# Optimization experiments

Hardware: AMD Instinct MI355X
Metric: run time of the kernel (lower is better)

Reference implementation:

```python
import jax, jax.numpy as jnp
import numpy as np

B, C, T = 8, 256, 4096
IC = C // 2  # inter_channels
BN_EPS = 1e-5


def setup_inputs() -> dict:
    key = jax.random.key(0)
    ks = jax.random.split(key, 12)
    s_in = 1.0 / np.sqrt(C)
    s_ic = 1.0 / np.sqrt(IC)
    return {
        "x": jax.random.normal(ks[0], (B, C, T), dtype=jnp.float32),
        "theta_w": jax.random.uniform(ks[1], (IC, C), jnp.float32, -s_in, s_in),
        "theta_b": jax.random.uniform(ks[2], (IC,), jnp.float32, -s_in, s_in),
        "phi_w": jax.random.uniform(ks[3], (IC, C), jnp.float32, -s_in, s_in),
        "phi_b": jax.random.uniform(ks[4], (IC,), jnp.float32, -s_in, s_in),
        "g_w": jax.random.uniform(ks[5], (IC, C), jnp.float32, -s_in, s_in),
        "g_b": jax.random.uniform(ks[6], (IC,), jnp.float32, -s_in, s_in),
        "w_w": jax.random.uniform(ks[7], (C, IC), jnp.float32, -s_ic, s_ic),
        "w_b": jax.random.uniform(ks[8], (C,), jnp.float32, -s_ic, s_ic),
        "bn_gamma": jax.random.normal(ks[9], (C,), dtype=jnp.float32),
        "bn_beta": jax.random.normal(ks[10], (C,), dtype=jnp.float32),
    }


def _conv1x1(w, b, inp):
    # Conv1d kernel_size=1 == per-position channel matmul
    return jnp.einsum('oc,bct->bot', w, inp) + b[None, :, None]


def _maxpool2(z):
    b, c, t = z.shape
    return z.reshape(b, c, t // 2, 2).max(axis=-1)


def reference(x, theta_w, theta_b, phi_w, phi_b, g_w, g_b, w_w, w_b, bn_gamma, bn_beta):
    theta_x = _conv1x1(theta_w, theta_b, x)              # (B, IC, T)
    phi_x = _maxpool2(_conv1x1(phi_w, phi_b, x))         # (B, IC, T/2)
    g_x = _maxpool2(_conv1x1(g_w, g_b, x))               # (B, IC, T/2)

    # f = theta^T @ phi ; softmax-free, divided by N = T/2
    f = jnp.einsum('bct,bcs->bts', theta_x, phi_x)       # (B, T, T/2)
    f_div_C = f / f.shape[-1]
    y = jnp.einsum('bts,bcs->bct', f_div_C, g_x)         # (B, IC, T)

    w_y = _conv1x1(w_w, w_b, y)                          # (B, C, T)
    # BatchNorm1d (training-mode batch statistics over batch+time)
    mean = w_y.mean(axis=(0, 2), keepdims=True)
    var = w_y.var(axis=(0, 2), keepdims=True)
    w_y = (w_y - mean) * jax.lax.rsqrt(var + BN_EPS)
    w_y = w_y * bn_gamma[None, :, None] + bn_beta[None, :, None]
    return w_y + x
```

## Files before the change

### kernel.cpp

```cpp
#include <hip/hip_runtime.h>
#include <hip/hip_bf16.h>

typedef __attribute__((ext_vector_type(8))) short short8;
typedef __attribute__((ext_vector_type(4))) short short4v;
typedef __attribute__((ext_vector_type(4))) float floatx4;
typedef unsigned int u32;

#define BB 8
#define CC 256
#define ICH 128
#define TT 4096
#define SS 2048
static constexpr float BN_EPS = 1e-5f;
static constexpr float INV_S  = 1.0f / 2048.0f;
static constexpr float INV_BT = 1.0f / 32768.0f;

typedef const __attribute__((address_space(1))) u32* gas_ptr;
typedef __attribute__((address_space(3))) u32* las_ptr;
__device__ __forceinline__ void gl_lds16(const void* g, void* l) {
    __builtin_amdgcn_global_load_lds((gas_ptr)g, (las_ptr)l, 16, 0, 0);
}

__global__ __launch_bounds__(256) void k0x_transpose(
    const float* __restrict__ x, __hip_bfloat16* __restrict__ xt,
    const float* __restrict__ phi_w, const float* __restrict__ g_w,
    __hip_bfloat16* __restrict__ Wf)
{
    if (blockIdx.z == 8) {
        if (blockIdx.y != 0) return;
        int idx = blockIdx.x * 256 + threadIdx.x;
        const float* src = (idx < 8192) ? (phi_w + (size_t)idx * 4)
                                        : (g_w + (size_t)(idx - 8192) * 4);
        float4 v = *(const float4*)src;
        alignas(8) __hip_bfloat16 t[4];
        t[0] = __float2bfloat16(v.x); t[1] = __float2bfloat16(v.y);
        t[2] = __float2bfloat16(v.z); t[3] = __float2bfloat16(v.w);
        *(short4v*)(Wf + (size_t)idx * 4) = *(const short4v*)t;
        return;
    }

    __shared__ float Tl[64][65];
    const int b = blockIdx.z, cb = blockIdx.y * 64, tb = blockIdx.x * 64;
    const int tid = threadIdx.x;
    #pragma unroll
    for (int it = 0; it < 4; ++it) {
        int idx = tid + 256 * it;
        int row = idx >> 4, c4 = idx & 15;
        float4 v = *(const float4*)(x + ((size_t)b * CC + cb + row) * TT + tb + c4 * 4);
        Tl[row][c4 * 4 + 0] = v.x; Tl[row][c4 * 4 + 1] = v.y;
        Tl[row][c4 * 4 + 2] = v.z; Tl[row][c4 * 4 + 3] = v.w;
    }
    __syncthreads();
    #pragma unroll
    for (int it = 0; it < 2; ++it) {
        int idx = tid + 256 * it;
        int trow = idx >> 3, ch = idx & 7;
        alignas(16) __hip_bfloat16 tmp[8];
        #pragma unroll
        for (int e = 0; e < 8; ++e) tmp[e] = __float2bfloat16(Tl[ch * 8 + e][trow]);
        *(short8*)(xt + ((size_t)b * TT + tb + trow) * CC + cb + ch * 8) = *(const short8*)tmp;
    }
}

__global__ __launch_bounds__(256) void k1_mfma(
    const __hip_bfloat16* __restrict__ Wf, const float* __restrict__ phi_b,
    const float* __restrict__ g_b, const __hip_bfloat16* __restrict__ xt,
    __hip_bfloat16* __restrict__ phi_g)
{
    __shared__ short lds[128 * 132];
    short* As = lds;
    short* Bs = lds + 128 * 64;

    const int b  = blockIdx.z;
    const int m0 = blockIdx.y * 128;
    const int tb = blockIdx.x * 128;
    const int s0 = blockIdx.x * 64;
    const int tid = threadIdx.x;
    const int w = tid >> 6, l = tid & 63;
    const int quad = l >> 4, lm = l & 15;
    const int wm = (w & 1) * 64, wn = (w >> 1) * 64;
    const int rs = l >> 3, cs = (l & 7) * 8;

    const __hip_bfloat16* Ap = Wf + (size_t)m0 * CC;
    const __hip_bfloat16* Bp = xt + ((size_t)b * TT + tb) * CC;

    floatx4 acc[4][4];
    #pragma unroll
    for (int i = 0; i < 4; ++i)
        #pragma unroll
        for (int j = 0; j < 4; ++j) acc[i][j] = (floatx4)0.f;

    for (int kc = 0; kc < 4; ++kc) {
        const int k0 = kc * 64;
        const int rbase = w * 32;
        #pragma unroll
        for (int t = 0; t < 4; ++t) {
            gl_lds16(Ap + (size_t)(rbase + t * 8 + rs) * CC + k0 + cs, &As[(rbase + t * 8) * 64]);
            gl_lds16(Bp + (size_t)(rbase + t * 8 + rs) * CC + k0 + cs, &Bs[(rbase + t * 8) * 64]);
        }
        __syncthreads();
        #pragma unroll
        for (int ks = 0; ks < 2; ++ks) {
            short8 a[4], bb[4];
            #pragma unroll
            for (int i = 0; i < 4; ++i)
                a[i] = *(const short8*)&As[(wm + i * 16 + lm) * 64 + ks * 32 + quad * 8];
            #pragma unroll
            for (int j = 0; j < 4; ++j)
                bb[j] = *(const short8*)&Bs[(wn + j * 16 + lm) * 64 + ks * 32 + quad * 8];
            #pragma unroll
            for (int i = 0; i < 4; ++i)
                #pragma unroll
                for (int j = 0; j < 4; ++j)
                    acc[i][j] = __builtin_amdgcn_mfma_f32_16x16x32_bf16(a[i], bb[j], acc[i][j], 0, 0, 0);
        }
        __syncthreads();
    }

    __hip_bfloat16* Out = (__hip_bfloat16*)lds;
    #pragma unroll
    for (int i = 0; i < 4; ++i)
        #pragma unroll
        for (int j = 0; j < 4; ++j)
            #pragma unroll
            for (int r = 0; r < 4; ++r)
                Out[(wm + i * 16 + quad * 4 + r) * 132 + wn + j * 16 + lm] =
                    __float2bfloat16(acc[i][j][r]);
    __syncthreads();
    #pragma unroll
    for (int it = 0; it < 4; ++it) {
        int idx = tid + 256 * it;
        int orow = idx >> 3, grp = idx & 7;
        int o = m0 + orow;
        float bias = (o < ICH) ? phi_b[o] : g_b[o - ICH];
        short8 v0 = *(const short8*)&Out[orow * 132 + grp * 16];
        short8 v1 = *(const short8*)&Out[orow * 132 + grp * 16 + 8];
        const __hip_bfloat16* p0 = (const __hip_bfloat16*)&v0;
        const __hip_bfloat16* p1 = (const __hip_bfloat16*)&v1;
        alignas(16) __hip_bfloat16 o8[8];
        #pragma unroll
        for (int e = 0; e < 4; ++e)
            o8[e] = __float2bfloat16(
                fmaxf(__bfloat162float(p0[2 * e]), __bfloat162float(p0[2 * e + 1])) + bias);
        #pragma unroll
        for (int e = 0; e < 4; ++e)
            o8[4 + e] = __float2bfloat16(
                fmaxf(__bfloat162float(p1[2 * e]), __bfloat162float(p1[2 * e + 1])) + bias);
        *(short8*)(phi_g + ((size_t)b * CC + o) * SS + s0 + grp * 8) = *(const short8*)o8;
    }
}

__global__ __launch_bounds__(256) void k2_mfma(
    const __hip_bfloat16* __restrict__ phi_g, float* __restrict__ Mpart)
{
    __shared__ short lds[2 * 128 * 64];
    short* As = lds;
    short* Bs = lds + 128 * 64;
    const int sc = blockIdx.x, b = blockIdx.y;
    const int tid = threadIdx.x;
    const int w = tid >> 6, l = tid & 63;
    const int quad = l >> 4, lm = l & 15;
    const int wm = (w & 1) * 64, wn = (w >> 1) * 64;
    const int rs = l >> 3, cs = (l & 7) * 8;

    const __hip_bfloat16* Ap = phi_g + (size_t)b * CC * SS + sc * 512;
    const __hip_bfloat16* Bp = Ap + (size_t)ICH * SS;

    floatx4 acc[4][4];
    #pragma unroll
    for (int i = 0; i < 4; ++i)
        #pragma unroll
        for (int j = 0; j < 4; ++j) acc[i][j] = (floatx4)0.f;

    for (int kc = 0; kc < 8; ++kc) {
        const int k0 = kc * 64;
        const int rbase = w * 32;
        #pragma unroll
        for (int t = 0; t < 4; ++t) {
            gl_lds16(Ap + (size_t)(rbase + t * 8 + rs) * SS + k0 + cs, &As[(rbase + t * 8) * 64]);
            gl_lds16(Bp + (size_t)(rbase + t * 8 + rs) * SS + k0 + cs, &Bs[(rbase + t * 8) * 64]);
        }
        __syncthreads();
        #pragma unroll
        for (int ks = 0; ks < 2; ++ks) {
            short8 a[4], bb[4];
            #pragma unroll
            for (int i = 0; i < 4; ++i)
                a[i] = *(const short8*)&As[(wm + i * 16 + lm) * 64 + ks * 32 + quad * 8];
            #pragma unroll
            for (int j = 0; j < 4; ++j)
                bb[j] = *(const short8*)&Bs[(wn + j * 16 + lm) * 64 + ks * 32 + quad * 8];
            #pragma unroll
            for (int i = 0; i < 4; ++i)
                #pragma unroll
                for (int j = 0; j < 4; ++j)
                    acc[i][j] = __builtin_amdgcn_mfma_f32_16x16x32_bf16(a[i], bb[j], acc[i][j], 0, 0, 0);
        }
        __syncthreads();
    }

    float* dst = Mpart + ((size_t)(b * 4 + sc)) * ICH * ICH;
    #pragma unroll
    for (int i = 0; i < 4; ++i)
        #pragma unroll
        for (int j = 0; j < 4; ++j)
            #pragma unroll
            for (int r = 0; r < 4; ++r)
                dst[(size_t)(wm + i * 16 + quad * 4 + r) * ICH + wn + j * 16 + lm] = acc[i][j][r];
}

__global__ __launch_bounds__(256) void k3a_kb(
    const float* __restrict__ w_w, const float* __restrict__ Mpart,
    float* __restrict__ Kb)
{
    __shared__ float Al[64][65];
    __shared__ float Bl[64][65];
    const int b = blockIdx.z;
    const int cob = blockIdx.y * 64;
    const int cpb = blockIdx.x * 64;
    const int tid = threadIdx.x;
    const int tx = tid & 15, ty = tid >> 4;

    float acc[4][4] = {};
    for (int kc2 = 0; kc2 < 2; ++kc2) {
        #pragma unroll
        for (int r = 0; r < 4; ++r) {
            int idx = tid + 256 * r;
            int row = idx >> 4, c4 = idx & 15;
            float4 v = *(const float4*)(w_w + (size_t)(cob + row) * ICH + kc2 * 64 + c4 * 4);
            Al[c4 * 4 + 0][row] = v.x; Al[c4 * 4 + 1][row] = v.y;
            Al[c4 * 4 + 2][row] = v.z; Al[c4 * 4 + 3][row] = v.w;
            float4 s = {0.f, 0.f, 0.f, 0.f};
            #pragma unroll
            for (int sc = 0; sc < 4; ++sc) {
                float4 m = *(const float4*)(Mpart + (((size_t)b * 4 + sc) * ICH + cpb + row) * ICH + kc2 * 64 + c4 * 4);
                s.x += m.x; s.y += m.y; s.z += m.z; s.w += m.w;
            }
            Bl[c4 * 4 + 0][row] = s.x; Bl[c4 * 4 + 1][row] = s.y;
            Bl[c4 * 4 + 2][row] = s.z; Bl[c4 * 4 + 3][row] = s.w;
        }
        __syncthreads();
        for (int k = 0; k < 64; ++k) {
            float av[4], bv[4];
            #pragma unroll
            for (int i = 0; i < 4; ++i) av[i] = Al[k][ty + 16 * i];
            #pragma unroll
            for (int j = 0; j < 4; ++j) bv[j] = Bl[k][tx + 16 * j];
            #pragma unroll
            for (int i = 0; i < 4; ++i)
                #pragma unroll
                for (int j = 0; j < 4; ++j) acc[i][j] += av[i] * bv[j];
        }
        __syncthreads();
    }
    #pragma unroll
    for (int i = 0; i < 4; ++i)
        #pragma unroll
        for (int j = 0; j < 4; ++j)
            Kb[((size_t)b * CC + cob + ty + 16 * i) * ICH + cpb + tx + 16 * j] = acc[i][j] * INV_S;
}

__global__ __launch_bounds__(256) void k3b_p(
    const float* __restrict__ Kb, const float* __restrict__ theta_w,
    const float* __restrict__ theta_b, const float* __restrict__ w_b,
    __hip_bfloat16* __restrict__ P, float* __restrict__ q)
{
    __shared__ float Al[64][65];
    __shared__ float Bl[64][128];
    const int b = blockIdx.z;
    const int cob = blockIdx.y * 64;
    const int cib = blockIdx.x * 128;
    const int tid = threadIdx.x;
    const int tx = tid & 15, ty = tid >> 4;

    float acc[4][8] = {};
    for (int kc2 = 0; kc2 < 2; ++kc2) {
        #pragma unroll
        for (int r = 0; r < 4; ++r) {
            int idx = tid + 256 * r;
            int row = idx >> 4, c4 = idx & 15;
            float4 v = *(const float4*)(Kb + ((size_t)b * CC + cob + row) * ICH + kc2 * 64 + c4 * 4);
            Al[c4 * 4 + 0][row] = v.x; Al[c4 * 4 + 1][row] = v.y;
            Al[c4 * 4 + 2][row] = v.z; Al[c4 * 4 + 3][row] = v.w;
        }
        #pragma unroll
        for (int r = 0; r < 8; ++r) {
            int idx = tid + 256 * r;
            int row = idx >> 5, c4 = idx & 31;
            *(float4*)(&Bl[row][c4 * 4]) =
                *(const float4*)(theta_w + (size_t)(kc2 * 64 + row) * CC + cib + c4 * 4);
        }
        __syncthreads();
        for (int k = 0; k < 64; ++k) {
            float av[4], bv[8];
            #pragma unroll
            for (int i = 0; i < 4; ++i) av[i] = Al[k][ty + 16 * i];
            #pragma unroll
            for (int j = 0; j < 8; ++j) bv[j] = Bl[k][tx + 16 * j];
            #pragma unroll
            for (int i = 0; i < 4; ++i)
                #pragma unroll
                for (int j = 0; j < 8; ++j) acc[i][j] += av[i] * bv[j];
        }
        __syncthreads();
    }
    #pragma unroll
    for (int i = 0; i < 4; ++i)
        #pragma unroll
        for (int j = 0; j < 8; ++j)
            P[((size_t)b * CC + cob + ty + 16 * i) * CC + cib + tx + 16 * j] =
                __float2bfloat16(acc[i][j]);

    if (blockIdx.x == 0 && tid < 64) {
        const float* kr = Kb + ((size_t)b * CC + cob + tid) * ICH;
        float s = w_b[cob + tid];
        #pragma unroll 8
        for (int c = 0; c < ICH; ++c) s += kr[c] * theta_b[c];
        q[b * CC + cob + tid] = s;
    }
}

__global__ __launch_bounds__(256) void k4_mfma(
    const __hip_bfloat16* __restrict__ P, const __hip_bfloat16* __restrict__ xt,
    const float* __restrict__ q, __hip_bfloat16* __restrict__ wy,
    float* __restrict__ pbuf)
{
    __shared__ short lds[128 * 132];
    __shared__ float pst1[4 * 64], pst2[4 * 64];
    short* As = lds;
    short* Bs = lds + 128 * 64;

    const int b  = blockIdx.z;
    const int m0 = blockIdx.y * 128;
    const int t0 = blockIdx.x * 128;
    const int tid = threadIdx.x;
    const int w = tid >> 6, l = tid & 63;
    const int quad = l >> 4, lm = l & 15;
    const int wm = (w & 1) * 64, wn = (w >> 1) * 64;
    const int rs = l >> 3, cs = (l & 7) * 8;

    const __hip_bfloat16* Ap = P + ((size_t)b * CC + m0) * CC;
    const __hip_bfloat16* Bp = xt + ((size_t)b * TT + t0) * CC;

    floatx4 acc[4][4];
    #pragma unroll
    for (int i = 0; i < 4; ++i)
        #pragma unroll
        for (int j = 0; j < 4; ++j) acc[i][j] = (floatx4)0.f;

    for (int kc = 0; kc < 4; ++kc) {
        const int k0 = kc * 64;
        const int rbase = w * 32;
        #pragma unroll
        for (int t = 0; t < 4; ++t) {
            gl_lds16(Ap + (size_t)(rbase + t * 8 + rs) * CC + k0 + cs, &As[(rbase + t * 8) * 64]);
            gl_lds16(Bp + (size_t)(rbase + t * 8 + rs) * CC + k0 + cs, &Bs[(rbase + t * 8) * 64]);
        }
        __syncthreads();
        #pragma unroll
        for (int ks = 0; ks < 2; ++ks) {
            short8 a[4], bb[4];
            #pragma unroll
            for (int i = 0; i < 4; ++i)
                a[i] = *(const short8*)&As[(wm + i * 16 + lm) * 64 + ks * 32 + quad * 8];
            #pragma unroll
            for (int j = 0; j < 4; ++j)
                bb[j] = *(const short8*)&Bs[(wn + j * 16 + lm) * 64 + ks * 32 + quad * 8];
            #pragma unroll
            for (int i = 0; i < 4; ++i)
                #pragma unroll
                for (int j = 0; j < 4; ++j)
                    acc[i][j] = __builtin_amdgcn_mfma_f32_16x16x32_bf16(a[i], bb[j], acc[i][j], 0, 0, 0);
        }
        __syncthreads();
    }

    #pragma unroll
    for (int i = 0; i < 4; ++i) {
        #pragma unroll
        for (int r = 0; r < 4; ++r) {
            int m = wm + i * 16 + quad * 4 + r;
            float bias = q[b * CC + m0 + m];
            float s1 = 0.f, s2 = 0.f;
            #pragma unroll
            for (int j = 0; j < 4; ++j) {
                float v = acc[i][j][r] + bias;
                s1 += v; s2 += v * v;
            }
            #pragma unroll
            for (int off = 1; off < 16; off <<= 1) {
                s1 += __shfl_xor(s1, off);
                s2 += __shfl_xor(s2, off);
            }
            if (lm == 0) {
                pst1[w * 64 + i * 16 + quad * 4 + r] = s1;
                pst2[w * 64 + i * 16 + quad * 4 + r] = s2;
            }
        }
    }

    __hip_bfloat16* Out = (__hip_bfloat16*)lds;
    #pragma unroll
    for (int i = 0; i < 4; ++i) {
        #pragma unroll
        for (int r = 0; r < 4; ++r) {
            int m = wm + i * 16 + quad * 4 + r;
            float bias = q[b * CC + m0 + m];
            #pragma unroll
            for (int j = 0; j < 4; ++j)
                Out[m * 132 + wn + j * 16 + lm] = __float2bfloat16(acc[i][j][r] + bias);
        }
    }
    __syncthreads();

    if (tid < 128) {
        int half = tid >> 6, k = tid & 63;
        float s1 = pst1[half * 64 + k] + pst1[(2 + half) * 64 + k];
        float s2 = pst2[half * 64 + k] + pst2[(2 + half) * 64 + k];
        size_t col = (size_t)b * 32 + blockIdx.x;
        pbuf[(size_t)(m0 + tid) * 256 + col] = s1;
        pbuf[65536 + (size_t)(m0 + tid) * 256 + col] = s2;
    }

    #pragma unroll
    for (int it = 0; it < 8; ++it) {
        int idx = tid + 256 * it;
        int row = idx >> 4, cg = idx & 15;
        *(short8*)(wy + ((size_t)b * CC + m0 + row) * TT + t0 + cg * 8) =
            *(const short8*)&Out[row * 132 + cg * 8];
    }
}

__global__ __launch_bounds__(256) void k5_bn(
    const float* __restrict__ pbuf, const float* __restrict__ gamma,
    const float* __restrict__ beta, float* __restrict__ coef)
{
    const int c = blockIdx.x, tid = threadIdx.x;
    float v1 = pbuf[(size_t)c * 256 + tid];
    float v2 = pbuf[65536 + (size_t)c * 256 + tid];
    #pragma unroll
    for (int off = 1; off < 64; off <<= 1) {
        v1 += __shfl_xor(v1, off);
        v2 += __shfl_xor(v2, off);
    }
    __shared__ float r1[4], r2[4];
    if ((tid & 63) == 0) { r1[tid >> 6] = v1; r2[tid >> 6] = v2; }
    __syncthreads();
    if (tid == 0) {
        float t1 = r1[0] + r1[1] + r1[2] + r1[3];
        float t2 = r2[0] + r2[1] + r2[2] + r2[3];
        float mean = t1 * INV_BT;
        float var  = t2 * INV_BT - mean * mean;
        float A = gamma[c] * rsqrtf(var + BN_EPS);
        coef[c] = A;
        coef[CC + c] = beta[c] - mean * A;
    }
}

__global__ __launch_bounds__(256) void k6_out(
    const __hip_bfloat16* __restrict__ wy, const __hip_bfloat16* __restrict__ xt,
    const float* __restrict__ coef, float* __restrict__ out)
{
    __shared__ float Fs[64][68];
    const int b = blockIdx.z, cb = blockIdx.y * 64, tb = blockIdx.x * 64;
    const int tid = threadIdx.x;

    {
        const int t = tid >> 2, cseg = (tid & 3) * 16;
        const __hip_bfloat16* src = xt + ((size_t)b * TT + tb + t) * CC + cb + cseg;
        short8 v0 = *(const short8*)src;
        short8 v1 = *(const short8*)(src + 8);
        const __hip_bfloat16* p0 = (const __hip_bfloat16*)&v0;
        const __hip_bfloat16* p1 = (const __hip_bfloat16*)&v1;
        #pragma unroll
        for (int e = 0; e < 8; ++e) Fs[t][cseg + e] = __bfloat162float(p0[e]);
        #pragma unroll
        for (int e = 0; e < 8; ++e) Fs[t][cseg + 8 + e] = __bfloat162float(p1[e]);
    }
    __syncthreads();

    const int c = tid >> 2, seg = (tid & 3) * 16;
    const float A = coef[cb + c], Bc = coef[CC + cb + c];
    const __hip_bfloat16* wsrc = wy + ((size_t)b * CC + cb + c) * TT + tb + seg;
    short8 w0 = *(const short8*)wsrc;
    short8 w1 = *(const short8*)(wsrc + 8);
    const __hip_bfloat16* q0 = (const __hip_bfloat16*)&w0;
    const __hip_bfloat16* q1 = (const __hip_bfloat16*)&w1;
    float* dst = out + ((size_t)b * CC + cb + c) * TT + tb + seg;
    #pragma unroll
    for (int e = 0; e < 8; ++e)
        dst[e] = __bfloat162float(q0[e]) * A + Bc + Fs[seg + e][c];
    #pragma unroll
    for (int e = 0; e < 8; ++e)
        dst[8 + e] = __bfloat162float(q1[e]) * A + Bc + Fs[seg + 8 + e][c];
}

extern "C" void kernel_launch(void* const* d_in, const int* in_sizes, int n_in,
                              void* d_out, int out_size, void* d_ws, size_t ws_size,
                              hipStream_t stream)
{
    const float* x        = (const float*)d_in[0];
    const float* theta_w  = (const float*)d_in[1];
    const float* theta_b  = (const float*)d_in[2];
    const float* phi_w    = (const float*)d_in[3];
    const float* phi_b    = (const float*)d_in[4];
    const float* g_w      = (const float*)d_in[5];
    const float* g_b      = (const float*)d_in[6];
    const float* w_w      = (const float*)d_in[7];
    const float* w_b      = (const float*)d_in[8];
    const float* bn_gamma = (const float*)d_in[9];
    const float* bn_beta  = (const float*)d_in[10];
    float* out = (float*)d_out;

    char* p = (char*)d_ws;
    __hip_bfloat16* xt    = (__hip_bfloat16*)p; p += (size_t)8388608 * 2;
    __hip_bfloat16* Wf    = (__hip_bfloat16*)p; p += (size_t)65536 * 2;
    __hip_bfloat16* phi_g = (__hip_bfloat16*)p; p += (size_t)4194304 * 2;
    __hip_bfloat16* P     = (__hip_bfloat16*)p; p += (size_t)524288 * 2;
    float* Mpart = (float*)p; p += (size_t)524288 * 4;
    float* Kb    = (float*)p; p += (size_t)262144 * 4;
    float* q     = (float*)p; p += (size_t)2048 * 4;
    __hip_bfloat16* wy = (__hip_bfloat16*)p; p += (size_t)8388608 * 2;
    float* pbuf  = (float*)p; p += (size_t)131072 * 4;
    float* coef  = (float*)p;

    k0x_transpose<<<dim3(64, 4, 9), 256, 0, stream>>>(x, xt, phi_w, g_w, Wf);
    k1_mfma<<<dim3(32, 2, 8), 256, 0, stream>>>(Wf, phi_b, g_b, xt, phi_g);
    k2_mfma<<<dim3(4, 8), 256, 0, stream>>>(phi_g, Mpart);
    k3a_kb<<<dim3(2, 4, 8), 256, 0, stream>>>(w_w, Mpart, Kb);
    k3b_p<<<dim3(2, 4, 8), 256, 0, stream>>>(Kb, theta_w, theta_b, w_b, P, q);
    k4_mfma<<<dim3(32, 2, 8), 256, 0, stream>>>(P, xt, q, wy, pbuf);
    k5_bn<<<dim3(256), 256, 0, stream>>>(pbuf, bn_gamma, bn_beta, coef);
    k6_out<<<dim3(64, 4, 8), 256, 0, stream>>>(wy, xt, coef, out);
}
```

Baseline: 180.5 us.

## Fuse mid-stage GEMMs into one persistent kernel with grid barriers and fold BN into output

Merges the phi·g^T reduction, the w_w·M product and the P/q construction into one 128-block kernel that uses atomic-counter grid barriers instead of separate launches. It also splits the reduction over S into 16 chunks instead of 4, raising block count from 32 to 128. The BN coefficient kernel is removed and each output block recomputes its channel statistics from pbuf, with 4 time tiles per block. This trades launch overhead for a spin-wait barrier that assumes all 128 blocks are co-resident, more Mpart traffic, and redundant BN reductions.

```diff
diff --git a/kernel.cpp b/kernel.cpp
--- a/kernel.cpp
+++ b/kernel.cpp
@@ -21,13 +21,27 @@
     __builtin_amdgcn_global_load_lds((gas_ptr)g, (las_ptr)l, 16, 0, 0);
 }
 
+__device__ __forceinline__ void grid_sync(int* bar, int target) {
+    __syncthreads();
+    if (threadIdx.x == 0) {
+        __threadfence();
+        atomicAdd(bar, 1);
+        while (__hip_atomic_load(bar, __ATOMIC_ACQUIRE,
+                                 __HIP_MEMORY_SCOPE_AGENT) < target)
+            __builtin_amdgcn_s_sleep(1);
+        __threadfence();
+    }
+    __syncthreads();
+}
+
 __global__ __launch_bounds__(256) void k0x_transpose(
     const float* __restrict__ x, __hip_bfloat16* __restrict__ xt,
     const float* __restrict__ phi_w, const float* __restrict__ g_w,
-    __hip_bfloat16* __restrict__ Wf)
+    __hip_bfloat16* __restrict__ Wf, int* __restrict__ bar)
 {
     if (blockIdx.z == 8) {
         if (blockIdx.y != 0) return;
+        if (blockIdx.x == 0 && threadIdx.x == 0) *bar = 0;
         int idx = blockIdx.x * 256 + threadIdx.x;
         const float* src = (idx < 8192) ? (phi_w + (size_t)idx * 4)
                                         : (g_w + (size_t)(idx - 8192) * 4);
@@ -150,173 +164,175 @@
     }
 }
 
-__global__ __launch_bounds__(256) void k2_mfma(
-    const __hip_bfloat16* __restrict__ phi_g, float* __restrict__ Mpart)
+__global__ __launch_bounds__(256) void kmid(
+    const __hip_bfloat16* __restrict__ phi_g, float* __restrict__ Mpart,
+    const float* __restrict__ w_w, float* __restrict__ Kb,
+    const float* __restrict__ theta_w, const float* __restrict__ theta_b,
+    const float* __restrict__ w_b, __hip_bfloat16* __restrict__ P,
+    float* __restrict__ q, int* __restrict__ bar)
 {
-    __shared__ short lds[2 * 128 * 64];
-    short* As = lds;
-    short* Bs = lds + 128 * 64;
-    const int sc = blockIdx.x, b = blockIdx.y;
+    __shared__ __align__(16) float ldsf[8512];
     const int tid = threadIdx.x;
-    const int w = tid >> 6, l = tid & 63;
-    const int quad = l >> 4, lm = l & 15;
-    const int wm = (w & 1) * 64, wn = (w >> 1) * 64;
-    const int rs = l >> 3, cs = (l & 7) * 8;
-
-    const __hip_bfloat16* Ap = phi_g + (size_t)b * CC * SS + sc * 512;
-    const __hip_bfloat16* Bp = Ap + (size_t)ICH * SS;
-
-    floatx4 acc[4][4];
-    #pragma unroll
-    for (int i = 0; i < 4; ++i)
-        #pragma unroll
-        for (int j = 0; j < 4; ++j) acc[i][j] = (floatx4)0.f;
-
-    for (int kc = 0; kc < 8; ++kc) {
-        const int k0 = kc * 64;
-        const int rbase = w * 32;
-        #pragma unroll
-        for (int t = 0; t < 4; ++t) {
-            gl_lds16(Ap + (size_t)(rbase + t * 8 + rs) * SS + k0 + cs, &As[(rbase + t * 8) * 64]);
-            gl_lds16(Bp + (size_t)(rbase + t * 8 + rs) * SS + k0 + cs, &Bs[(rbase + t * 8) * 64]);
-        }
-        __syncthreads();
-        #pragma unroll
-        for (int ks = 0; ks < 2; ++ks) {
-            short8 a[4], bb[4];
-            #pragma unroll
-            for (int i = 0; i < 4; ++i)
-                a[i] = *(const short8*)&As[(wm + i * 16 + lm) * 64 + ks * 32 + quad * 8];
+    const int bid = blockIdx.x;
+
+    {
+        short* As = (short*)ldsf;
+        short* Bs = As + 128 * 64;
+        const int sc = bid & 15, b = bid >> 4;
+        const int w = tid >> 6, l = tid & 63;
+        const int quad = l >> 4, lm = l & 15;
+        const int wm = (w & 1) * 64, wn = (w >> 1) * 64;
+        const int rs = l >> 3, cs = (l & 7) * 8;
+        const __hip_bfloat16* Ap = phi_g + (size_t)b * CC * SS + sc * 128;
+        const __hip_bfloat16* Bp = Ap + (size_t)ICH * SS;
+
+        floatx4 acc[4][4];
+        #pragma unroll
+        for (int i = 0; i < 4; ++i)
+            #pragma unroll
+            for (int j = 0; j < 4; ++j) acc[i][j] = (floatx4)0.f;
+
+        for (int kc = 0; kc < 2; ++kc) {
+            const int k0 = kc * 64;
+            const int rbase = w * 32;
+            #pragma unroll
+            for (int t = 0; t < 4; ++t) {
+                gl_lds16(Ap + (size_t)(rbase + t * 8 + rs) * SS + k0 + cs, &As[(rbase + t * 8) * 64]);
+                gl_lds16(Bp + (size_t)(rbase + t * 8 + rs) * SS + k0 + cs, &Bs[(rbase + t * 8) * 64]);
+            }
+            __syncthreads();
+            #pragma unroll
+            for (int ks = 0; ks < 2; ++ks) {
+                short8 a[4], bb[4];
+                #pragma unroll
+                for (int i = 0; i < 4; ++i)
+                    a[i] = *(const short8*)&As[(wm + i * 16 + lm) * 64 + ks * 32 + quad * 8];
+                #pragma unroll
+                for (int j = 0; j < 4; ++j)
+                    bb[j] = *(const short8*)&Bs[(wn + j * 16 + lm) * 64 + ks * 32 + quad * 8];
+                #pragma unroll
+                for (int i = 0; i < 4; ++i)
+                    #pragma unroll
+                    for (int j = 0; j < 4; ++j)
+                        acc[i][j] = __builtin_amdgcn_mfma_f32_16x16x32_bf16(a[i], bb[j], acc[i][j], 0, 0, 0);
+            }
+            __syncthreads();
+        }
+
+        float* dst = Mpart + ((size_t)(b * 16 + sc)) * ICH * ICH;
+        #pragma unroll
+        for (int i = 0; i < 4; ++i)
             #pragma unroll
             for (int j = 0; j < 4; ++j)
-                bb[j] = *(const short8*)&Bs[(wn + j * 16 + lm) * 64 + ks * 32 + quad * 8];
-            #pragma unroll
-            for (int i = 0; i < 4; ++i)
-                #pragma unroll
-                for (int j = 0; j < 4; ++j)
-                    acc[i][j] = __builtin_amdgcn_mfma_f32_16x16x32_bf16(a[i], bb[j], acc[i][j], 0, 0, 0);
-        }
-        __syncthreads();
-    }
-
-    float* dst = Mpart + ((size_t)(b * 4 + sc)) * ICH * ICH;
-    #pragma unroll
-    for (int i = 0; i < 4; ++i)
-        #pragma unroll
-        for (int j = 0; j < 4; ++j)
-            #pragma unroll
-            for (int r = 0; r < 4; ++r)
-                dst[(size_t)(wm + i * 16 + quad * 4 + r) * ICH + wn + j * 16 + lm] = acc[i][j][r];
-}
-
-__global__ __launch_bounds__(256) void k3a_kb(
-    const float* __restrict__ w_w, const float* __restrict__ Mpart,
-    float* __restrict__ Kb)
-{
-    __shared__ float Al[64][65];
-    __shared__ float Bl[64][65];
-    const int b = blockIdx.z;
-    const int cob = blockIdx.y * 64;
-    const int cpb = blockIdx.x * 64;
-    const int tid = threadIdx.x;
-    const int tx = tid & 15, ty = tid >> 4;
-
-    float acc[4][4] = {};
-    for (int kc2 = 0; kc2 < 2; ++kc2) {
-        #pragma unroll
-        for (int r = 0; r < 4; ++r) {
-            int idx = tid + 256 * r;
-            int row = idx >> 4, c4 = idx & 15;
-            float4 v = *(const float4*)(w_w + (size_t)(cob + row) * ICH + kc2 * 64 + c4 * 4);
-            Al[c4 * 4 + 0][row] = v.x; Al[c4 * 4 + 1][row] = v.y;
-            Al[c4 * 4 + 2][row] = v.z; Al[c4 * 4 + 3][row] = v.w;
-            float4 s = {0.f, 0.f, 0.f, 0.f};
-            #pragma unroll
-            for (int sc = 0; sc < 4; ++sc) {
-                float4 m = *(const float4*)(Mpart + (((size_t)b * 4 + sc) * ICH + cpb + row) * ICH + kc2 * 64 + c4 * 4);
-                s.x += m.x; s.y += m.y; s.z += m.z; s.w += m.w;
-            }
-            Bl[c4 * 4 + 0][row] = s.x; Bl[c4 * 4 + 1][row] = s.y;
-            Bl[c4 * 4 + 2][row] = s.z; Bl[c4 * 4 + 3][row] = s.w;
-        }
-        __syncthreads();
-        for (int k = 0; k < 64; ++k) {
-            float av[4], bv[4];
-            #pragma unroll
-            for (int i = 0; i < 4; ++i) av[i] = Al[k][ty + 16 * i];
-            #pragma unroll
-            for (int j = 0; j < 4; ++j) bv[j] = Bl[k][tx + 16 * j];
-            #pragma unroll
-            for (int i = 0; i < 4; ++i)
-                #pragma unroll
-                for (int j = 0; j < 4; ++j) acc[i][j] += av[i] * bv[j];
-        }
-        __syncthreads();
-    }
-    #pragma unroll
-    for (int i = 0; i < 4; ++i)
-        #pragma unroll
-        for (int j = 0; j < 4; ++j)
-            Kb[((size_t)b * CC + cob + ty + 16 * i) * ICH + cpb + tx + 16 * j] = acc[i][j] * INV_S;
-}
-
-__global__ __launch_bounds__(256) void k3b_p(
-    const float* __restrict__ Kb, const float* __restrict__ theta_w,
-    const float* __restrict__ theta_b, const float* __restrict__ w_b,
-    __hip_bfloat16* __restrict__ P, float* __restrict__ q)
-{
-    __shared__ float Al[64][65];
-    __shared__ float Bl[64][128];
-    const int b = blockIdx.z;
-    const int cob = blockIdx.y * 64;
-    const int cib = blockIdx.x * 128;
-    const int tid = threadIdx.x;
-    const int tx = tid & 15, ty = tid >> 4;
-
-    float acc[4][8] = {};
-    for (int kc2 = 0; kc2 < 2; ++kc2) {
-        #pragma unroll
-        for (int r = 0; r < 4; ++r) {
-            int idx = tid + 256 * r;
-            int row = idx >> 4, c4 = idx & 15;
-            float4 v = *(const float4*)(Kb + ((size_t)b * CC + cob + row) * ICH + kc2 * 64 + c4 * 4);
-            Al[c4 * 4 + 0][row] = v.x; Al[c4 * 4 + 1][row] = v.y;
-            Al[c4 * 4 + 2][row] = v.z; Al[c4 * 4 + 3][row] = v.w;
-        }
-        #pragma unroll
-        for (int r = 0; r < 8; ++r) {
-            int idx = tid + 256 * r;
-            int row = idx >> 5, c4 = idx & 31;
-            *(float4*)(&Bl[row][c4 * 4]) =
-                *(const float4*)(theta_w + (size_t)(kc2 * 64 + row) * CC + cib + c4 * 4);
-        }
-        __syncthreads();
-        for (int k = 0; k < 64; ++k) {
-            float av[4], bv[8];
-            #pragma unroll
-            for (int i = 0; i < 4; ++i) av[i] = Al[k][ty + 16 * i];
-            #pragma unroll
-            for (int j = 0; j < 8; ++j) bv[j] = Bl[k][tx + 16 * j];
-            #pragma unroll
-            for (int i = 0; i < 4; ++i)
-                #pragma unroll
-                for (int j = 0; j < 8; ++j) acc[i][j] += av[i] * bv[j];
-        }
-        __syncthreads();
-    }
-    #pragma unroll
-    for (int i = 0; i < 4; ++i)
-        #pragma unroll
-        for (int j = 0; j < 8; ++j)
-            P[((size_t)b * CC + cob + ty + 16 * i) * CC + cib + tx + 16 * j] =
-                __float2bfloat16(acc[i][j]);
-
-    if (blockIdx.x == 0 && tid < 64) {
-        const float* kr = Kb + ((size_t)b * CC + cob + tid) * ICH;
-        float s = w_b[cob + tid];
-        #pragma unroll 8
-        for (int c = 0; c < ICH; ++c) s += kr[c] * theta_b[c];
-        q[b * CC + cob + tid] = s;
+                #pragma unroll
+                for (int r = 0; r < 4; ++r)
+                    dst[(size_t)(wm + i * 16 + quad * 4 + r) * ICH + wn + j * 16 + lm] = acc[i][j][r];
+    }
+
+    grid_sync(bar, 128);
+
+    if (bid < 64) {
+        float (*Al)[65] = (float (*)[65])ldsf;
+        float (*Bl)[65] = Al + 64;
+        const int b   = bid >> 3;
+        const int cob = ((bid >> 1) & 3) * 64;
+        const int cpb = (bid & 1) * 64;
+        const int tx = tid & 15, ty = tid >> 4;
+
+        float acc[4][4] = {};
+        for (int kc2 = 0; kc2 < 2; ++kc2) {
+            #pragma unroll
+            for (int r = 0; r < 4; ++r) {
+                int idx = tid + 256 * r;
+                int row = idx >> 4, c4 = idx & 15;
+                float4 v = *(const float4*)(w_w + (size_t)(cob + row) * ICH + kc2 * 64 + c4 * 4);
+                Al[c4 * 4 + 0][row] = v.x; Al[c4 * 4 + 1][row] = v.y;
+                Al[c4 * 4 + 2][row] = v.z; Al[c4 * 4 + 3][row] = v.w;
+                float4 s = {0.f, 0.f, 0.f, 0.f};
+                #pragma unroll
+                for (int sc = 0; sc < 16; ++sc) {
+                    float4 m = *(const float4*)(Mpart + (((size_t)b * 16 + sc) * ICH + cpb + row) * ICH + kc2 * 64 + c4 * 4);
+                    s.x += m.x; s.y += m.y; s.z += m.z; s.w += m.w;
+                }
+                Bl[c4 * 4 + 0][row] = s.x; Bl[c4 * 4 + 1][row] = s.y;
+                Bl[c4 * 4 + 2][row] = s.z; Bl[c4 * 4 + 3][row] = s.w;
+            }
+            __syncthreads();
+            for (int k = 0; k < 64; ++k) {
+                float av[4], bv[4];
+                #pragma unroll
+                for (int i = 0; i < 4; ++i) av[i] = Al[k][ty + 16 * i];
+                #pragma unroll
+                for (int j = 0; j < 4; ++j) bv[j] = Bl[k][tx + 16 * j];
+                #pragma unroll
+                for (int i = 0; i < 4; ++i)
+                    #pragma unroll
+                    for (int j = 0; j < 4; ++j) acc[i][j] += av[i] * bv[j];
+            }
+            __syncthreads();
+        }
+        #pragma unroll
+        for (int i = 0; i < 4; ++i)
+            #pragma unroll
+            for (int j = 0; j < 4; ++j)
+                Kb[((size_t)b * CC + cob + ty + 16 * i) * ICH + cpb + tx + 16 * j] = acc[i][j] * INV_S;
+    }
+
+    grid_sync(bar, 256);
+
+    {
+        float (*Al)[65] = (float (*)[65])ldsf;
+        float (*Bl)[68] = (float (*)[68])(ldsf + 64 * 65);
+        const int b   = bid >> 4;
+        const int cob = ((bid >> 2) & 3) * 64;
+        const int cib = (bid & 3) * 64;
+        const int tx = tid & 15, ty = tid >> 4;
+
+        float acc[4][4] = {};
+        for (int kc2 = 0; kc2 < 2; ++kc2) {
+            #pragma unroll
+            for (int r = 0; r < 4; ++r) {
+                int idx = tid + 256 * r;
+                int row = idx >> 4, c4 = idx & 15;
+                float4 v = *(const float4*)(Kb + ((size_t)b * CC + cob + row) * ICH + kc2 * 64 + c4 * 4);
+                Al[c4 * 4 + 0][row] = v.x; Al[c4 * 4 + 1][row] = v.y;
+                Al[c4 * 4 + 2][row] = v.z; Al[c4 * 4 + 3][row] = v.w;
+            }
+            #pragma unroll
+            for (int r = 0; r < 4; ++r) {
+                int idx = tid + 256 * r;
+                int row = idx >> 4, c4 = idx & 15;
+                *(float4*)(&Bl[row][c4 * 4]) =
+                    *(const float4*)(theta_w + (size_t)(kc2 * 64 + row) * CC + cib + c4 * 4);
+            }
+            __syncthreads();
+            for (int k = 0; k < 64; ++k) {
+                float av[4], bv[4];
+                #pragma unroll
+                for (int i = 0; i < 4; ++i) av[i] = Al[k][ty + 16 * i];
+                #pragma unroll
+                for (int j = 0; j < 4; ++j) bv[j] = Bl[k][tx + 16 * j];
+                #pragma unroll
+                for (int i = 0; i < 4; ++i)
+                    #pragma unroll
+                    for (int j = 0; j < 4; ++j) acc[i][j] += av[i] * bv[j];
+            }
+            __syncthreads();
+        }
+        #pragma unroll
+        for (int i = 0; i < 4; ++i)
+            #pragma unroll
+            for (int j = 0; j < 4; ++j)
+                P[((size_t)b * CC + cob + ty + 16 * i) * CC + cib + tx + 16 * j] =
+                    __float2bfloat16(acc[i][j]);
+
+        if ((bid & 3) == 0 && tid < 64) {
+            const float* kr = Kb + ((size_t)b * CC + cob + tid) * ICH;
+            float s = w_b[cob + tid];
+            #pragma unroll 8
+            for (int c = 0; c < ICH; ++c) s += kr[c] * theta_b[c];
+            q[b * CC + cob + tid] = s;
+        }
     }
 }
 
@@ -431,68 +447,72 @@
     }
 }
 
-__global__ __launch_bounds__(256) void k5_bn(
-    const float* __restrict__ pbuf, const float* __restrict__ gamma,
-    const float* __restrict__ beta, float* __restrict__ coef)
-{
-    const int c = blockIdx.x, tid = threadIdx.x;
-    float v1 = pbuf[(size_t)c * 256 + tid];
-    float v2 = pbuf[65536 + (size_t)c * 256 + tid];
-    #pragma unroll
-    for (int off = 1; off < 64; off <<= 1) {
-        v1 += __shfl_xor(v1, off);
-        v2 += __shfl_xor(v2, off);
-    }
-    __shared__ float r1[4], r2[4];
-    if ((tid & 63) == 0) { r1[tid >> 6] = v1; r2[tid >> 6] = v2; }
-    __syncthreads();
-    if (tid == 0) {
-        float t1 = r1[0] + r1[1] + r1[2] + r1[3];
-        float t2 = r2[0] + r2[1] + r2[2] + r2[3];
-        float mean = t1 * INV_BT;
-        float var  = t2 * INV_BT - mean * mean;
-        float A = gamma[c] * rsqrtf(var + BN_EPS);
-        coef[c] = A;
-        coef[CC + c] = beta[c] - mean * A;
-    }
-}
-
 __global__ __launch_bounds__(256) void k6_out(
     const __hip_bfloat16* __restrict__ wy, const __hip_bfloat16* __restrict__ xt,
-    const float* __restrict__ coef, float* __restrict__ out)
+    const float* __restrict__ pbuf, const float* __restrict__ gamma,
+    const float* __restrict__ beta, float* __restrict__ out)
 {
     __shared__ float Fs[64][68];
-    const int b = blockIdx.z, cb = blockIdx.y * 64, tb = blockIdx.x * 64;
+    __shared__ float cA[64], cB[64];
+    const int b = blockIdx.z, cb = blockIdx.y * 64, tb0 = blockIdx.x * 256;
     const int tid = threadIdx.x;
 
     {
-        const int t = tid >> 2, cseg = (tid & 3) * 16;
-        const __hip_bfloat16* src = xt + ((size_t)b * TT + tb + t) * CC + cb + cseg;
-        short8 v0 = *(const short8*)src;
-        short8 v1 = *(const short8*)(src + 8);
-        const __hip_bfloat16* p0 = (const __hip_bfloat16*)&v0;
-        const __hip_bfloat16* p1 = (const __hip_bfloat16*)&v1;
-        #pragma unroll
-        for (int e = 0; e < 8; ++e) Fs[t][cseg + e] = __bfloat162float(p0[e]);
-        #pragma unroll
-        for (int e = 0; e < 8; ++e) Fs[t][cseg + 8 + e] = __bfloat162float(p1[e]);
-    }
-    __syncthreads();
-
-    const int c = tid >> 2, seg = (tid & 3) * 16;
-    const float A = coef[cb + c], Bc = coef[CC + cb + c];
-    const __hip_bfloat16* wsrc = wy + ((size_t)b * CC + cb + c) * TT + tb + seg;
-    short8 w0 = *(const short8*)wsrc;
-    short8 w1 = *(const short8*)(wsrc + 8);
-    const __hip_bfloat16* q0 = (const __hip_bfloat16*)&w0;
-    const __hip_bfloat16* q1 = (const __hip_bfloat16*)&w1;
-    float* dst = out + ((size_t)b * CC + cb + c) * TT + tb + seg;
-    #pragma unroll
-    for (int e = 0; e < 8; ++e)
-        dst[e] = __bfloat162float(q0[e]) * A + Bc + Fs[seg + e][c];
-    #pragma unroll
-    for (int e = 0; e < 8; ++e)
-        dst[8 + e] = __bfloat162float(q1[e]) * A + Bc + Fs[seg + 8 + e][c];
+        const int ch = tid >> 2, qtr = tid & 3;
+        const float* p1 = pbuf + (size_t)(cb + ch) * 256 + qtr * 64;
+        const float* p2 = p1 + 65536;
+        float s1 = 0.f, s2 = 0.f;
+        #pragma unroll
+        for (int e = 0; e < 16; ++e) {
+            float4 a = *(const float4*)(p1 + e * 4);
+            float4 c = *(const float4*)(p2 + e * 4);
+            s1 += a.x + a.y + a.z + a.w;
+            s2 += c.x + c.y + c.z + c.w;
+        }
+        s1 += __shfl_xor(s1, 1); s1 += __shfl_xor(s1, 2);
+        s2 += __shfl_xor(s2, 1); s2 += __shfl_xor(s2, 2);
+        if (qtr == 0) {
+            float mean = s1 * INV_BT;
+            float var  = s2 * INV_BT - mean * mean;
+            float A = gamma[cb + ch] * rsqrtf(var + BN_EPS);
+            cA[ch] = A;
+            cB[ch] = beta[cb + ch] - mean * A;
+        }
+    }
+
+    for (int tt = 0; tt < 4; ++tt) {
+        const int tb = tb0 + tt * 64;
+        __syncthreads();
+        {
+            const int t = tid >> 2, cseg = (tid & 3) * 16;
+            const __hip_bfloat16* src = xt + ((size_t)b * TT + tb + t) * CC + cb + cseg;
+            short8 v0 = *(const short8*)src;
+            short8 v1 = *(const short8*)(src + 8);
+            const __hip_bfloat16* p0 = (const __hip_bfloat16*)&v0;
+            const __hip_bfloat16* p1 = (const __hip_bfloat16*)&v1;
+            #pragma unroll
+            for (int e = 0; e < 8; ++e) Fs[t][cseg + e] = __bfloat162float(p0[e]);
+            #pragma unroll
+            for (int e = 0; e < 8; ++e) Fs[t][cseg + 8 + e] = __bfloat162float(p1[e]);
+        }
+        __syncthreads();
+        {
+            const int c = tid >> 2, seg = (tid & 3) * 16;
+            const float A = cA[c], Bc = cB[c];
+            const __hip_bfloat16* wsrc = wy + ((size_t)b * CC + cb + c) * TT + tb + seg;
+            short8 w0 = *(const short8*)wsrc;
+            short8 w1 = *(const short8*)(wsrc + 8);
+            const __hip_bfloat16* q0 = (const __hip_bfloat16*)&w0;
+            const __hip_bfloat16* q1 = (const __hip_bfloat16*)&w1;
+            float* dst = out + ((size_t)b * CC + cb + c) * TT + tb + seg;
+            #pragma unroll
+            for (int e = 0; e < 8; ++e)
+                dst[e] = __bfloat162float(q0[e]) * A + Bc + Fs[seg + e][c];
+            #pragma unroll
+            for (int e = 0; e < 8; ++e)
+                dst[8 + e] = __bfloat162float(q1[e]) * A + Bc + Fs[seg + 8 + e][c];
+        }
+    }
 }
 
 extern "C" void kernel_launch(void* const* d_in, const int* in_sizes, int n_in,
@@ -517,19 +537,16 @@
     __hip_bfloat16* Wf    = (__hip_bfloat16*)p; p += (size_t)65536 * 2;
     __hip_bfloat16* phi_g = (__hip_bfloat16*)p; p += (size_t)4194304 * 2;
     __hip_bfloat16* P     = (__hip_bfloat16*)p; p += (size_t)524288 * 2;
-    float* Mpart = (float*)p; p += (size_t)524288 * 4;
+    float* Mpart = (float*)p; p += (size_t)2097152 * 4;
     float* Kb    = (float*)p; p += (size_t)262144 * 4;
     float* q     = (float*)p; p += (size_t)2048 * 4;
     __hip_bfloat16* wy = (__hip_bfloat16*)p; p += (size_t)8388608 * 2;
     float* pbuf  = (float*)p; p += (size_t)131072 * 4;
-    float* coef  = (float*)p;
-
-    k0x_transpose<<<dim3(64, 4, 9), 256, 0, stream>>>(x, xt, phi_w, g_w, Wf);
+    int* bar     = (int*)p;
+
+    k0x_transpose<<<dim3(64, 4, 9), 256, 0, stream>>>(x, xt, phi_w, g_w, Wf, bar);
     k1_mfma<<<dim3(32, 2, 8), 256, 0, stream>>>(Wf, phi_b, g_b, xt, phi_g);
-    k2_mfma<<<dim3(4, 8), 256, 0, stream>>>(phi_g, Mpart);
-    k3a_kb<<<dim3(2, 4, 8), 256, 0, stream>>>(w_w, Mpart, Kb);
-    k3b_p<<<dim3(2, 4, 8), 256, 0, stream>>>(Kb, theta_w, theta_b, w_b, P, q);
+    kmid<<<dim3(128), 256, 0, stream>>>(phi_g, Mpart, w_w, Kb, theta_w, theta_b, w_b, P, q, bar);
     k4_mfma<<<dim3(32, 2, 8), 256, 0, stream>>>(P, xt, q, wy, pbuf);
-    k5_bn<<<dim3(256), 256, 0, stream>>>(pbuf, bn_gamma, bn_beta, coef);
-    k6_out<<<dim3(64, 4, 8), 256, 0, stream>>>(wy, xt, coef, out);
-}
+    k6_out<<<dim3(16, 4, 8), 256, 0, stream>>>(wy, xt, pbuf, bn_gamma, bn_beta, out);
+}
```

New measurement: 263.7 us. 1.46x slower.
